# Kernel optimization log

Measured on AMD Instinct MI355X. Metric: run time of the kernel, lower is better.

## Reference

```python
import jax, jax.numpy as jnp
import numpy as np

B, S, D_IN, D_HEAD = 4, 4096, 1024, 64

def setup_inputs() -> dict:
    key = jax.random.key(0)
    k1, k2, k3, k4 = jax.random.split(key, 4)
    scale = 0.02
    return {
        "input_vectors": jax.random.normal(k1, (B, S, D_IN), dtype=jnp.float32),
        "Wq": jax.random.normal(k2, (D_IN, D_HEAD), dtype=jnp.float32) * scale,
        "Wk": jax.random.normal(k3, (D_IN, D_HEAD), dtype=jnp.float32) * scale,
        "Wv": jax.random.normal(k4, (D_IN, D_HEAD), dtype=jnp.float32) * scale,
    }

def reference(input_vectors, Wq, Wk, Wv):
    # QKV projections (Linear with no bias): [B,S,d_in] @ [d_in,d_head]
    q = input_vectors @ Wq  # [B,S,H]
    k = input_vectors @ Wk
    v = input_vectors @ Wv
    n = input_vectors.shape[1]
    # causal attention scores: [B,S,S]
    scores = jnp.einsum('bqh,bkh->bqk', q, k)
    causal = jnp.tril(jnp.ones((n, n), dtype=bool))  # True = keep
    scores = jnp.where(causal, scores, -jnp.inf)
    scale = k.shape[-1] ** -0.5
    attn = jax.nn.softmax(scores * scale, axis=-1)
    return jnp.einsum('bqk,bkh->bqh', attn, v)
```

## Files before the change

### kernel.cpp

```cpp
#include <hip/hip_runtime.h>
#include <stdint.h>

#define SEQ   4096
#define DHEAD 64
#define DIN   1024

typedef __attribute__((ext_vector_type(8))) short bf16x8;
typedef __attribute__((ext_vector_type(4))) float floatx4;
typedef __attribute__((ext_vector_type(4))) unsigned short ushortx4;

#if __has_builtin(__builtin_amdgcn_exp2f)
#define EXP2(x) __builtin_amdgcn_exp2f(x)
#else
#define EXP2(x) exp2f(x)
#endif

__device__ __forceinline__ unsigned short f2bf(float f) {
    union { float f; unsigned int u; } v; v.f = f;
    unsigned int u = v.u + 0x7fffu + ((v.u >> 16) & 1u);
    return (unsigned short)(u >> 16);
}
__device__ __forceinline__ float bf2f(unsigned short h) {
    union { unsigned int u; float f; } v; v.u = ((unsigned int)h) << 16;
    return v.f;
}

__global__ void wt_prep(const float* __restrict__ Wq, const float* __restrict__ Wk,
                        const float* __restrict__ Wv, unsigned short* __restrict__ WT) {
    int idx = blockIdx.x * 256 + threadIdx.x;
    int k   = idx & 1023;
    int n   = (idx >> 10) & 63;
    int mat = idx >> 16;
    const float* W = (mat == 0) ? Wq : ((mat == 1) ? Wk : Wv);
    WT[idx] = f2bf(W[k * 64 + n]);
}

#define QSCALE 0.18033688011112042f
__launch_bounds__(256, 4)
__global__ void proj_qkv(const float* __restrict__ X, const unsigned short* __restrict__ WT,
                         unsigned short* __restrict__ qb, unsigned short* __restrict__ kb,
                         unsigned short* __restrict__ vb) {
    __shared__ __align__(16) float          Xl[16 * 64];
    __shared__ __align__(16) unsigned short Wl[192 * 64];
    const int tid = threadIdx.x;
    const int wave = tid >> 6, lane = tid & 63;
    const int quad = lane >> 4, l16 = lane & 15;
    const int row0 = blockIdx.x * 16;
    const int m = l16;

    floatx4 acc[3];
#pragma unroll
    for (int i = 0; i < 3; i++) acc[i] = (floatx4){0.f, 0.f, 0.f, 0.f};

    floatx4 xpre;
    floatx4 wpre[6];

    const int xu = tid, xr = xu >> 4, xc = (xu & 15) ^ (xr & 15);
    int wu[6], wr[6], wc[6];
#pragma unroll
    for (int i = 0; i < 6; i++) {
        wu[i] = (wave * 6 + i) * 64 + lane;
        wr[i] = wu[i] >> 3;
        wc[i] = (wu[i] & 7) ^ (wr[i] & 7);
    }

    auto issue = [&](int k0) {
        xpre = *(const floatx4*)(X + (size_t)(row0 + xr) * DIN + k0 + xc * 4);
#pragma unroll
        for (int i = 0; i < 6; i++)
            wpre[i] = *(const floatx4*)(WT + (size_t)wr[i] * 1024 + k0 + wc[i] * 8);
    };

    issue(0);
    for (int kc = 0; kc < 16; kc++) {
        __syncthreads();
        *(floatx4*)&Xl[xu * 4] = xpre;
#pragma unroll
        for (int i = 0; i < 6; i++)
            *(floatx4*)&Wl[wu[i] * 8] = wpre[i];
        __syncthreads();
        if (kc < 15) issue((kc + 1) * 64);

        bf16x8 af[2];
#pragma unroll
        for (int ks = 0; ks < 2; ks++) {
            floatx4 x0 = *(const floatx4*)&Xl[m * 64 + ((ks * 8 + quad * 2 + 0) ^ m) * 4];
            floatx4 x1 = *(const floatx4*)&Xl[m * 64 + ((ks * 8 + quad * 2 + 1) ^ m) * 4];
#pragma unroll
            for (int j = 0; j < 4; j++) {
                af[ks][j]     = (short)f2bf(x0[j]);
                af[ks][j + 4] = (short)f2bf(x1[j]);
            }
        }
#pragma unroll
        for (int i = 0; i < 3; i++) {
            const int nrow = (wave * 3 + i) * 16 + l16;
#pragma unroll
            for (int ks = 0; ks < 2; ks++) {
                const int c = ks * 4 + quad;
                bf16x8 bfrag = *(const bf16x8*)&Wl[nrow * 64 + (c ^ (nrow & 7)) * 8];
                acc[i] = __builtin_amdgcn_mfma_f32_16x16x32_bf16(af[ks], bfrag, acc[i], 0, 0, 0);
            }
        }
    }
#pragma unroll
    for (int i = 0; i < 3; i++) {
        const int nt = wave * 3 + i;
        const int mat = nt >> 2;
        const int col = (nt & 3) * 16 + l16;
#pragma unroll
        for (int r = 0; r < 4; r++) {
            const int orow = row0 + quad * 4 + r;
            float v = acc[i][r];
            if (mat == 0) {
                qb[(size_t)orow * 64 + col] = f2bf(v * QSCALE);
            } else if (mat == 1) {
                kb[(size_t)orow * 64 + col] = f2bf(v);
            } else {
                int b = orow >> 12, s = orow & 4095;
                vb[((size_t)b * 64 + col) * SEQ + s] = f2bf(v);
            }
        }
    }
}

__launch_bounds__(256, 4)
__global__ void attn(const unsigned short* __restrict__ qb, const unsigned short* __restrict__ kb,
                     const unsigned short* __restrict__ vb, unsigned short* __restrict__ opart,
                     float* __restrict__ lpart) {
    __shared__ __align__(16) unsigned short Kl[64 * 64];
    __shared__ __align__(16) unsigned short Vl[64 * 64];
    __shared__ __align__(16) unsigned short Pl[4][16 * 72];

    const int bid = blockIdx.x;
    const int batch = bid & 3;
    const int mm = bid >> 2;
    const int idx = mm & 63, g = mm >> 6;
    const int rank = (g == 0) ? (255 - idx) : (g == 1) ? (128 + idx)
                   : (g == 2) ? (127 - idx) : idx;
    const int qt = rank >> 2, s = rank & 3;
    const int q0 = qt * 64;
    const int T = qt + 1;
    const int ktlo = (T * s) >> 2;
    const int kthi = (T * (s + 1)) >> 2;

    const int tid = threadIdx.x;
    const int wave = tid >> 6, lane = tid & 63;
    const int quad = lane >> 4, l16 = lane & 15;

    const unsigned short* qrow = qb + (size_t)(batch * SEQ + q0 + wave * 16 + l16) * 64;
    bf16x8 qa[2];
    qa[0] = *(const bf16x8*)(qrow + quad * 8);
    qa[1] = *(const bf16x8*)(qrow + 32 + quad * 8);

    floatx4 o[4];
#pragma unroll
    for (int i = 0; i < 4; i++) o[i] = (floatx4){0.f, 0.f, 0.f, 0.f};
    float lrow[4] = {0.f, 0.f, 0.f, 0.f};

    const unsigned short* kbase = kb + (size_t)batch * SEQ * 64;
    const unsigned short* vbase = vb + (size_t)batch * 64 * SEQ;

    int ku[2], kr[2], kc_[2], vu[2], vd[2], vc[2];
#pragma unroll
    for (int i = 0; i < 2; i++) {
        ku[i] = i * 256 + tid; kr[i] = ku[i] >> 3; kc_[i] = (ku[i] & 7) ^ (kr[i] & 7);
        vu[i] = i * 256 + tid; vd[i] = vu[i] >> 3; vc[i] = (vu[i] & 7) ^ (vd[i] & 7);
    }
    floatx4 kpre[2], vpre[2];
    auto issue = [&](int k0) {
#pragma unroll
        for (int i = 0; i < 2; i++)
            kpre[i] = *(const floatx4*)(kbase + (size_t)(k0 + kr[i]) * 64 + kc_[i] * 8);
#pragma unroll
        for (int i = 0; i < 2; i++)
            vpre[i] = *(const floatx4*)(vbase + (size_t)vd[i] * SEQ + k0 + vc[i] * 8);
    };

    if (ktlo < kthi) issue(ktlo * 64);
    for (int kt = ktlo; kt < kthi; kt++) {
        __syncthreads();
#pragma unroll
        for (int i = 0; i < 2; i++) *(floatx4*)&Kl[ku[i] * 8] = kpre[i];
#pragma unroll
        for (int i = 0; i < 2; i++) *(floatx4*)&Vl[vu[i] * 8] = vpre[i];
        __syncthreads();
        if (kt + 1 < kthi) issue((kt + 1) * 64);

        const int k0 = kt * 64;
        floatx4 sc[4];
#pragma unroll
        for (int nt = 0; nt < 4; nt++) {
            sc[nt] = (floatx4){0.f, 0.f, 0.f, 0.f};
            const int key = nt * 16 + l16;
#pragma unroll
            for (int ks = 0; ks < 2; ks++) {
                const int c = ks * 4 + quad;
                bf16x8 bk = *(const bf16x8*)&Kl[key * 64 + (c ^ (key & 7)) * 8];
                sc[nt] = __builtin_amdgcn_mfma_f32_16x16x32_bf16(qa[ks], bk, sc[nt], 0, 0, 0);
            }
        }
        if (kt == T - 1) {
#pragma unroll
            for (int nt = 0; nt < 4; nt++) {
                const int col = k0 + nt * 16 + l16;
#pragma unroll
                for (int r = 0; r < 4; r++) {
                    const int rowg = q0 + wave * 16 + quad * 4 + r;
                    if (col > rowg) sc[nt][r] = -1e30f;
                }
            }
        }
        unsigned short* P = &Pl[wave][0];
#pragma unroll
        for (int r = 0; r < 4; r++) {
#pragma unroll
            for (int nt = 0; nt < 4; nt++) {
                float p = EXP2(sc[nt][r]);
                lrow[r] += p;
                P[(quad * 4 + r) * 72 + nt * 16 + l16] = f2bf(p);
            }
        }
        bf16x8 pa[2];
        pa[0] = *(const bf16x8*)&P[l16 * 72 + quad * 8];
        pa[1] = *(const bf16x8*)&P[l16 * 72 + 32 + quad * 8];
#pragma unroll
        for (int nt = 0; nt < 4; nt++) {
            const int d = nt * 16 + l16;
#pragma unroll
            for (int ks = 0; ks < 2; ks++) {
                const int c = ks * 4 + quad;
                bf16x8 bv = *(const bf16x8*)&Vl[d * 64 + (c ^ (d & 7)) * 8];
                o[nt] = __builtin_amdgcn_mfma_f32_16x16x32_bf16(pa[ks], bv, o[nt], 0, 0, 0);
            }
        }
    }

    unsigned short* ob = opart + (size_t)s * (4 * SEQ * 64)
                       + (size_t)(batch * SEQ + q0 + wave * 16) * 64;
    float* lb = lpart + (size_t)s * (4 * SEQ) + (size_t)(batch * SEQ + q0 + wave * 16);
#pragma unroll
    for (int r = 0; r < 4; r++) {
        float l = lrow[r];
        l += __shfl_xor(l, 1);
        l += __shfl_xor(l, 2);
        l += __shfl_xor(l, 4);
        l += __shfl_xor(l, 8);
#pragma unroll
        for (int nt = 0; nt < 4; nt++)
            ob[(quad * 4 + r) * 64 + nt * 16 + l16] = f2bf(o[nt][r]);
        if (l16 == 0) lb[quad * 4 + r] = l;
    }
}

__global__ void merge(const unsigned short* __restrict__ opart, const float* __restrict__ lpart,
                      float* __restrict__ out) {
    int idx = blockIdx.x * 256 + threadIdx.x;
    int row = idx >> 4, c4 = idx & 15;
    float l = lpart[row] + lpart[4 * SEQ + row] + lpart[8 * SEQ + row] + lpart[12 * SEQ + row];
    float inv = 1.f / l;
    floatx4 acc = (floatx4){0.f, 0.f, 0.f, 0.f};
#pragma unroll
    for (int s = 0; s < 4; s++) {
        ushortx4 u = *(const ushortx4*)(opart + (size_t)s * (4 * SEQ * 64)
                                        + (size_t)row * 64 + c4 * 4);
#pragma unroll
        for (int j = 0; j < 4; j++) acc[j] += bf2f(u[j]);
    }
    acc *= inv;
    *(floatx4*)(out + (size_t)row * 64 + c4 * 4) = acc;
}

extern "C" void kernel_launch(void* const* d_in, const int* in_sizes, int n_in,
                              void* d_out, int out_size, void* d_ws, size_t ws_size,
                              hipStream_t stream) {
    const float* X  = (const float*)d_in[0];
    const float* Wq = (const float*)d_in[1];
    const float* Wk = (const float*)d_in[2];
    const float* Wv = (const float*)d_in[3];
    float* out = (float*)d_out;
    char* ws = (char*)d_ws;
    unsigned short* WT = (unsigned short*)ws;
    unsigned short* qb = (unsigned short*)(ws + 393216);
    unsigned short* kb = (unsigned short*)(ws + 393216 + 2097152);
    unsigned short* vb = (unsigned short*)(ws + 393216 + 2 * 2097152);
    unsigned short* opart = (unsigned short*)(ws + 393216 + 3 * 2097152);
    float* lpart = (float*)(ws + 393216 + 3 * 2097152 + 8388608);

    hipLaunchKernelGGL(wt_prep,  dim3(768),  dim3(256), 0, stream, Wq, Wk, Wv, WT);
    hipLaunchKernelGGL(proj_qkv, dim3(1024), dim3(256), 0, stream, X, WT, qb, kb, vb);
    hipLaunchKernelGGL(attn,     dim3(1024), dim3(256), 0, stream, qb, kb, vb, opart, lpart);
    hipLaunchKernelGGL(merge,    dim3(1024), dim3(256), 0, stream, opart, lpart, out);
}
```

Measured before the change: 144.9 us.

## Enlarge projection and attention tiles, double-buffer LDS, and transpose P via DPP

The projection kernel now handles 64 rows per 512-thread block, so each weight tile staged in LDS is reused across four row strips. The attention kernel now covers 128 query rows per block, two 16-row tiles per wave, so each K/V tile is reused twice. Both kernels double-buffer LDS, which drops one barrier per iteration and overlaps global prefetch with compute. The P write is reorganised with DPP lane exchanges into packed 64-bit stores with truncated bf16, and masking is limited to diagonal tiles. The trade-offs are more registers and LDS per block, lower occupancy, half as many attention blocks, and truncation instead of rounding for P.

```diff
diff --git a/kernel.cpp b/kernel.cpp
--- a/kernel.cpp
+++ b/kernel.cpp
@@ -2,7 +2,6 @@
 #include <stdint.h>
 
 #define SEQ   4096
-#define DHEAD 64
 #define DIN   1024
 
 typedef __attribute__((ext_vector_type(8))) short bf16x8;
@@ -24,68 +23,83 @@
     union { unsigned int u; float f; } v; v.u = ((unsigned int)h) << 16;
     return v.f;
 }
+__device__ __forceinline__ float uasf(unsigned int u) {
+    union { unsigned int u; float f; } v; v.u = u; return v.f;
+}
+__device__ __forceinline__ unsigned int fasu(float f) {
+    union { float f; unsigned int u; } v; v.f = f; return v.u;
+}
+__device__ __forceinline__ float dpp_xor1(float x) {
+    return uasf((unsigned)__builtin_amdgcn_mov_dpp((int)fasu(x), 0xB1, 0xF, 0xF, true));
+}
+__device__ __forceinline__ float dpp_xor2(float x) {
+    return uasf((unsigned)__builtin_amdgcn_mov_dpp((int)fasu(x), 0x4E, 0xF, 0xF, true));
+}
 
 __global__ void wt_prep(const float* __restrict__ Wq, const float* __restrict__ Wk,
                         const float* __restrict__ Wv, unsigned short* __restrict__ WT) {
     int idx = blockIdx.x * 256 + threadIdx.x;
-    int k   = idx & 1023;
-    int n   = (idx >> 10) & 63;
+    int n   = idx & 63;
+    int k   = (idx >> 6) & 1023;
     int mat = idx >> 16;
     const float* W = (mat == 0) ? Wq : ((mat == 1) ? Wk : Wv);
-    WT[idx] = f2bf(W[k * 64 + n]);
+    WT[(size_t)(mat * 64 + n) * 1024 + k] = f2bf(W[k * 64 + n]);
 }
 
 #define QSCALE 0.18033688011112042f
-__launch_bounds__(256, 4)
+__launch_bounds__(512, 2)
 __global__ void proj_qkv(const float* __restrict__ X, const unsigned short* __restrict__ WT,
                          unsigned short* __restrict__ qb, unsigned short* __restrict__ kb,
                          unsigned short* __restrict__ vb) {
-    __shared__ __align__(16) float          Xl[16 * 64];
-    __shared__ __align__(16) unsigned short Wl[192 * 64];
+    __shared__ __align__(16) float          X0[64 * 64], X1[64 * 64];
+    __shared__ __align__(16) unsigned short W0[192 * 64], W1[192 * 64];
     const int tid = threadIdx.x;
     const int wave = tid >> 6, lane = tid & 63;
     const int quad = lane >> 4, l16 = lane & 15;
-    const int row0 = blockIdx.x * 16;
-    const int m = l16;
-
-    floatx4 acc[3];
-#pragma unroll
-    for (int i = 0; i < 3; i++) acc[i] = (floatx4){0.f, 0.f, 0.f, 0.f};
-
-    floatx4 xpre;
-    floatx4 wpre[6];
-
-    const int xu = tid, xr = xu >> 4, xc = (xu & 15) ^ (xr & 15);
-    int wu[6], wr[6], wc[6];
-#pragma unroll
-    for (int i = 0; i < 6; i++) {
-        wu[i] = (wave * 6 + i) * 64 + lane;
-        wr[i] = wu[i] >> 3;
-        wc[i] = (wu[i] & 7) ^ (wr[i] & 7);
-    }
-
+    const int strip = wave >> 1;
+    const int cg = wave & 1;
+    const int row0 = blockIdx.x * 64;
+    const int m = strip * 16 + l16;
+
+    floatx4 acc[6];
+#pragma unroll
+    for (int i = 0; i < 6; i++) acc[i] = (floatx4){0.f, 0.f, 0.f, 0.f};
+
+    int xu[2], xr[2], xc[2], wu[3], wr[3], wc[3];
+#pragma unroll
+    for (int i = 0; i < 2; i++) {
+        xu[i] = i * 512 + tid; xr[i] = xu[i] >> 4; xc[i] = (xu[i] & 15) ^ (xr[i] & 15);
+    }
+#pragma unroll
+    for (int i = 0; i < 3; i++) {
+        wu[i] = i * 512 + tid; wr[i] = wu[i] >> 3; wc[i] = (wu[i] & 7) ^ (wr[i] & 7);
+    }
+    floatx4 xpre[2], wpre[3];
     auto issue = [&](int k0) {
-        xpre = *(const floatx4*)(X + (size_t)(row0 + xr) * DIN + k0 + xc * 4);
-#pragma unroll
-        for (int i = 0; i < 6; i++)
+#pragma unroll
+        for (int i = 0; i < 2; i++)
+            xpre[i] = *(const floatx4*)(X + (size_t)(row0 + xr[i]) * DIN + k0 + xc[i] * 4);
+#pragma unroll
+        for (int i = 0; i < 3; i++)
             wpre[i] = *(const floatx4*)(WT + (size_t)wr[i] * 1024 + k0 + wc[i] * 8);
     };
 
     issue(0);
     for (int kc = 0; kc < 16; kc++) {
+        float*          Xd = (kc & 1) ? X1 : X0;
+        unsigned short* Wd = (kc & 1) ? W1 : W0;
+#pragma unroll
+        for (int i = 0; i < 2; i++) *(floatx4*)&Xd[xu[i] * 4] = xpre[i];
+#pragma unroll
+        for (int i = 0; i < 3; i++) *(floatx4*)&Wd[wu[i] * 8] = wpre[i];
+        if (kc < 15) issue((kc + 1) * 64);
         __syncthreads();
-        *(floatx4*)&Xl[xu * 4] = xpre;
-#pragma unroll
-        for (int i = 0; i < 6; i++)
-            *(floatx4*)&Wl[wu[i] * 8] = wpre[i];
-        __syncthreads();
-        if (kc < 15) issue((kc + 1) * 64);
 
         bf16x8 af[2];
 #pragma unroll
         for (int ks = 0; ks < 2; ks++) {
-            floatx4 x0 = *(const floatx4*)&Xl[m * 64 + ((ks * 8 + quad * 2 + 0) ^ m) * 4];
-            floatx4 x1 = *(const floatx4*)&Xl[m * 64 + ((ks * 8 + quad * 2 + 1) ^ m) * 4];
+            floatx4 x0 = *(const floatx4*)&Xd[m * 64 + ((ks * 8 + quad * 2 + 0) ^ (m & 15)) * 4];
+            floatx4 x1 = *(const floatx4*)&Xd[m * 64 + ((ks * 8 + quad * 2 + 1) ^ (m & 15)) * 4];
 #pragma unroll
             for (int j = 0; j < 4; j++) {
                 af[ks][j]     = (short)f2bf(x0[j]);
@@ -93,70 +107,71 @@
             }
         }
 #pragma unroll
-        for (int i = 0; i < 3; i++) {
-            const int nrow = (wave * 3 + i) * 16 + l16;
+        for (int i = 0; i < 6; i++) {
+            const int nrow = (cg * 6 + i) * 16 + l16;
 #pragma unroll
             for (int ks = 0; ks < 2; ks++) {
                 const int c = ks * 4 + quad;
-                bf16x8 bfrag = *(const bf16x8*)&Wl[nrow * 64 + (c ^ (nrow & 7)) * 8];
+                bf16x8 bfrag = *(const bf16x8*)&Wd[nrow * 64 + (c ^ (nrow & 7)) * 8];
                 acc[i] = __builtin_amdgcn_mfma_f32_16x16x32_bf16(af[ks], bfrag, acc[i], 0, 0, 0);
             }
         }
     }
 #pragma unroll
-    for (int i = 0; i < 3; i++) {
-        const int nt = wave * 3 + i;
+    for (int i = 0; i < 6; i++) {
+        const int nt = cg * 6 + i;
         const int mat = nt >> 2;
         const int col = (nt & 3) * 16 + l16;
 #pragma unroll
         for (int r = 0; r < 4; r++) {
-            const int orow = row0 + quad * 4 + r;
+            const int orow = row0 + strip * 16 + quad * 4 + r;
             float v = acc[i][r];
             if (mat == 0) {
                 qb[(size_t)orow * 64 + col] = f2bf(v * QSCALE);
             } else if (mat == 1) {
                 kb[(size_t)orow * 64 + col] = f2bf(v);
             } else {
-                int b = orow >> 12, s = orow & 4095;
-                vb[((size_t)b * 64 + col) * SEQ + s] = f2bf(v);
-            }
-        }
-    }
-}
-
-__launch_bounds__(256, 4)
+                int b = orow >> 12, sq = orow & 4095;
+                vb[((size_t)b * 64 + col) * SEQ + sq] = f2bf(v);
+            }
+        }
+    }
+}
+
+__launch_bounds__(256, 2)
 __global__ void attn(const unsigned short* __restrict__ qb, const unsigned short* __restrict__ kb,
                      const unsigned short* __restrict__ vb, unsigned short* __restrict__ opart,
                      float* __restrict__ lpart) {
-    __shared__ __align__(16) unsigned short Kl[64 * 64];
-    __shared__ __align__(16) unsigned short Vl[64 * 64];
-    __shared__ __align__(16) unsigned short Pl[4][16 * 72];
+    __shared__ __align__(16) unsigned short K0[64 * 64], K1[64 * 64];
+    __shared__ __align__(16) unsigned short V0[64 * 64], V1[64 * 64];
+    __shared__ __align__(16) unsigned short Pl[4][32 * 72];
 
     const int bid = blockIdx.x;
     const int batch = bid & 3;
     const int mm = bid >> 2;
-    const int idx = mm & 63, g = mm >> 6;
-    const int rank = (g == 0) ? (255 - idx) : (g == 1) ? (128 + idx)
-                   : (g == 2) ? (127 - idx) : idx;
+    const int rank = (bid < 256) ? (127 - mm) : (mm - 64);
     const int qt = rank >> 2, s = rank & 3;
-    const int q0 = qt * 64;
-    const int T = qt + 1;
-    const int ktlo = (T * s) >> 2;
-    const int kthi = (T * (s + 1)) >> 2;
+    const int q0 = qt * 128;
+    const int T = 2 * qt + 2;
+    const int ktlo = (T * s) >> 2, kthi = (T * (s + 1)) >> 2;
 
     const int tid = threadIdx.x;
     const int wave = tid >> 6, lane = tid & 63;
     const int quad = lane >> 4, l16 = lane & 15;
 
-    const unsigned short* qrow = qb + (size_t)(batch * SEQ + q0 + wave * 16 + l16) * 64;
-    bf16x8 qa[2];
-    qa[0] = *(const bf16x8*)(qrow + quad * 8);
-    qa[1] = *(const bf16x8*)(qrow + 32 + quad * 8);
-
-    floatx4 o[4];
-#pragma unroll
-    for (int i = 0; i < 4; i++) o[i] = (floatx4){0.f, 0.f, 0.f, 0.f};
-    float lrow[4] = {0.f, 0.f, 0.f, 0.f};
+    bf16x8 qa[2][2];
+#pragma unroll
+    for (int rt = 0; rt < 2; rt++) {
+        const unsigned short* qr = qb + (size_t)(batch * SEQ + q0 + wave * 32 + rt * 16 + l16) * 64;
+        qa[rt][0] = *(const bf16x8*)(qr + quad * 8);
+        qa[rt][1] = *(const bf16x8*)(qr + 32 + quad * 8);
+    }
+    floatx4 o[2][4];
+#pragma unroll
+    for (int rt = 0; rt < 2; rt++)
+#pragma unroll
+        for (int nt = 0; nt < 4; nt++) o[rt][nt] = (floatx4){0.f, 0.f, 0.f, 0.f};
+    float lsum[2] = {0.f, 0.f};
 
     const unsigned short* kbase = kb + (size_t)batch * SEQ * 64;
     const unsigned short* vbase = vb + (size_t)batch * 64 * SEQ;
@@ -179,77 +194,93 @@
 
     if (ktlo < kthi) issue(ktlo * 64);
     for (int kt = ktlo; kt < kthi; kt++) {
+        unsigned short* Kd = (kt & 1) ? K1 : K0;
+        unsigned short* Vd = (kt & 1) ? V1 : V0;
+#pragma unroll
+        for (int i = 0; i < 2; i++) *(floatx4*)&Kd[ku[i] * 8] = kpre[i];
+#pragma unroll
+        for (int i = 0; i < 2; i++) *(floatx4*)&Vd[vu[i] * 8] = vpre[i];
+        if (kt + 1 < kthi) issue((kt + 1) * 64);
         __syncthreads();
-#pragma unroll
-        for (int i = 0; i < 2; i++) *(floatx4*)&Kl[ku[i] * 8] = kpre[i];
-#pragma unroll
-        for (int i = 0; i < 2; i++) *(floatx4*)&Vl[vu[i] * 8] = vpre[i];
-        __syncthreads();
-        if (kt + 1 < kthi) issue((kt + 1) * 64);
 
         const int k0 = kt * 64;
-        floatx4 sc[4];
-#pragma unroll
-        for (int nt = 0; nt < 4; nt++) {
-            sc[nt] = (floatx4){0.f, 0.f, 0.f, 0.f};
-            const int key = nt * 16 + l16;
-#pragma unroll
-            for (int ks = 0; ks < 2; ks++) {
-                const int c = ks * 4 + quad;
-                bf16x8 bk = *(const bf16x8*)&Kl[key * 64 + (c ^ (key & 7)) * 8];
-                sc[nt] = __builtin_amdgcn_mfma_f32_16x16x32_bf16(qa[ks], bk, sc[nt], 0, 0, 0);
-            }
-        }
-        if (kt == T - 1) {
+        const bool domask = (k0 + 63) > (q0 + wave * 32);
+        unsigned short* P = &Pl[wave][0];
+#pragma unroll
+        for (int rt = 0; rt < 2; rt++) {
+            floatx4 sc[4];
 #pragma unroll
             for (int nt = 0; nt < 4; nt++) {
-                const int col = k0 + nt * 16 + l16;
-#pragma unroll
-                for (int r = 0; r < 4; r++) {
-                    const int rowg = q0 + wave * 16 + quad * 4 + r;
-                    if (col > rowg) sc[nt][r] = -1e30f;
+                sc[nt] = (floatx4){0.f, 0.f, 0.f, 0.f};
+                const int key = nt * 16 + l16;
+#pragma unroll
+                for (int ks = 0; ks < 2; ks++) {
+                    const int c = ks * 4 + quad;
+                    bf16x8 bk = *(const bf16x8*)&Kd[key * 64 + (c ^ (key & 7)) * 8];
+                    sc[nt] = __builtin_amdgcn_mfma_f32_16x16x32_bf16(qa[rt][ks], bk, sc[nt], 0, 0, 0);
                 }
             }
-        }
-        unsigned short* P = &Pl[wave][0];
-#pragma unroll
-        for (int r = 0; r < 4; r++) {
+            if (domask) {
+#pragma unroll
+                for (int nt = 0; nt < 4; nt++) {
+                    const int col = k0 + nt * 16 + l16;
+#pragma unroll
+                    for (int r = 0; r < 4; r++) {
+                        const int rowg = q0 + wave * 32 + rt * 16 + quad * 4 + r;
+                        if (col > rowg) sc[nt][r] = -1e30f;
+                    }
+                }
+            }
 #pragma unroll
             for (int nt = 0; nt < 4; nt++) {
-                float p = EXP2(sc[nt][r]);
-                lrow[r] += p;
-                P[(quad * 4 + r) * 72 + nt * 16 + l16] = f2bf(p);
-            }
-        }
-        bf16x8 pa[2];
-        pa[0] = *(const bf16x8*)&P[l16 * 72 + quad * 8];
-        pa[1] = *(const bf16x8*)&P[l16 * 72 + 32 + quad * 8];
-#pragma unroll
-        for (int nt = 0; nt < 4; nt++) {
-            const int d = nt * 16 + l16;
-#pragma unroll
-            for (int ks = 0; ks < 2; ks++) {
-                const int c = ks * 4 + quad;
-                bf16x8 bv = *(const bf16x8*)&Vl[d * 64 + (c ^ (d & 7)) * 8];
-                o[nt] = __builtin_amdgcn_mfma_f32_16x16x32_bf16(pa[ks], bv, o[nt], 0, 0, 0);
+                float v0 = EXP2(sc[nt][0]), v1 = EXP2(sc[nt][1]);
+                float v2 = EXP2(sc[nt][2]), v3 = EXP2(sc[nt][3]);
+                float t0 = dpp_xor2(v0), t1 = dpp_xor2(v1), t2 = dpp_xor2(v2), t3 = dpp_xor2(v3);
+                if (lane & 2) { v0 = t2; v1 = t3; } else { v2 = t0; v3 = t1; }
+                t0 = dpp_xor1(v0); t1 = dpp_xor1(v1); t2 = dpp_xor1(v2); t3 = dpp_xor1(v3);
+                if (lane & 1) { v0 = t1; v2 = t3; } else { v1 = t0; v3 = t2; }
+                unsigned int u0 = fasu(v0) & 0xffff0000u, u1 = fasu(v1) & 0xffff0000u;
+                unsigned int u2 = fasu(v2) & 0xffff0000u, u3 = fasu(v3) & 0xffff0000u;
+                lsum[rt] += (uasf(u0) + uasf(u1)) + (uasf(u2) + uasf(u3));
+                uint2 w;
+                w.x = (u0 >> 16) | u1;
+                w.y = (u2 >> 16) | u3;
+                const int prow = rt * 16 + quad * 4 + (lane & 3);
+                const int pcol = nt * 16 + (l16 >> 2) * 4;
+                *(uint2*)&P[prow * 72 + pcol] = w;
+            }
+        }
+#pragma unroll
+        for (int ks = 0; ks < 2; ks++) {
+            bf16x8 pa[2];
+#pragma unroll
+            for (int rt = 0; rt < 2; rt++)
+                pa[rt] = *(const bf16x8*)&P[(rt * 16 + l16) * 72 + ks * 32 + quad * 8];
+#pragma unroll
+            for (int nt = 0; nt < 4; nt++) {
+                const int d = nt * 16 + l16;
+                bf16x8 bv = *(const bf16x8*)&Vd[d * 64 + (((ks * 4 + quad)) ^ (d & 7)) * 8];
+#pragma unroll
+                for (int rt = 0; rt < 2; rt++)
+                    o[rt][nt] = __builtin_amdgcn_mfma_f32_16x16x32_bf16(pa[rt], bv, o[rt][nt], 0, 0, 0);
             }
         }
     }
 
     unsigned short* ob = opart + (size_t)s * (4 * SEQ * 64)
-                       + (size_t)(batch * SEQ + q0 + wave * 16) * 64;
-    float* lb = lpart + (size_t)s * (4 * SEQ) + (size_t)(batch * SEQ + q0 + wave * 16);
-#pragma unroll
-    for (int r = 0; r < 4; r++) {
-        float l = lrow[r];
-        l += __shfl_xor(l, 1);
-        l += __shfl_xor(l, 2);
+                       + (size_t)(batch * SEQ + q0 + wave * 32) * 64;
+    float* lb = lpart + (size_t)s * (4 * SEQ) + (size_t)(batch * SEQ + q0 + wave * 32);
+#pragma unroll
+    for (int rt = 0; rt < 2; rt++) {
+        float l = lsum[rt];
         l += __shfl_xor(l, 4);
         l += __shfl_xor(l, 8);
 #pragma unroll
         for (int nt = 0; nt < 4; nt++)
-            ob[(quad * 4 + r) * 64 + nt * 16 + l16] = f2bf(o[nt][r]);
-        if (l16 == 0) lb[quad * 4 + r] = l;
+#pragma unroll
+            for (int r = 0; r < 4; r++)
+                ob[(rt * 16 + quad * 4 + r) * 64 + nt * 16 + l16] = f2bf(o[rt][nt][r]);
+        if ((l16 >> 2) == 0) lb[rt * 16 + quad * 4 + (l16 & 3)] = l;
     }
 }
 
@@ -287,8 +318,8 @@
     unsigned short* opart = (unsigned short*)(ws + 393216 + 3 * 2097152);
     float* lpart = (float*)(ws + 393216 + 3 * 2097152 + 8388608);
 
-    hipLaunchKernelGGL(wt_prep,  dim3(768),  dim3(256), 0, stream, Wq, Wk, Wv, WT);
-    hipLaunchKernelGGL(proj_qkv, dim3(1024), dim3(256), 0, stream, X, WT, qb, kb, vb);
-    hipLaunchKernelGGL(attn,     dim3(1024), dim3(256), 0, stream, qb, kb, vb, opart, lpart);
+    hipLaunchKernelGGL(wt_prep,  dim3(768), dim3(256), 0, stream, Wq, Wk, Wv, WT);
+    hipLaunchKernelGGL(proj_qkv, dim3(256), dim3(512), 0, stream, X, WT, qb, kb, vb);
+    hipLaunchKernelGGL(attn,     dim3(512), dim3(256), 0, stream, qb, kb, vb, opart, lpart);
     hipLaunchKernelGGL(merge,    dim3(1024), dim3(256), 0, stream, opart, lpart, out);
 }
```

Result: faster. 139.9 us (-3.5%).
